# Optimization experiments

Measured on AMD Instinct MI355X. Metric: run time of the kernel, lower is better.

## Reference

```python
import jax, jax.numpy as jnp
import numpy as np

B, C, H, W = 4, 384, 128, 128
HEADS = 8
EPS = 1e-12  # torch F.normalize default eps


def setup_inputs() -> dict:
    key = jax.random.key(0)
    k1, k2, k3, k4 = jax.random.split(key, 4)
    in1 = jax.random.normal(k1, (B, C, H, W), dtype=jnp.float32)
    in2 = jax.random.normal(k2, (B, C, H, W), dtype=jnp.float32)
    temperature = jnp.ones((HEADS, 1, 1), dtype=jnp.float32)
    proj_w = jax.random.normal(k3, (C, C), dtype=jnp.float32) * (1.0 / np.sqrt(C))
    proj_b = jax.random.normal(k4, (C,), dtype=jnp.float32) * 0.01
    return {"in1": in1, "in2": in2, "temperature": temperature,
            "proj_w": proj_w, "proj_b": proj_b}


def _l2norm_last(x):
    # torch F.normalize(dim=-1): x / max(||x||_2, eps)
    n = jnp.sqrt(jnp.sum(x * x, axis=-1, keepdims=True))
    return x / jnp.maximum(n, EPS)


def reference(in1, in2, temperature, proj_w, proj_b):
    b, c, h, w = in1.shape
    hd = c // HEADS  # per-head channels
    # b (head c) h w -> b head c (h w)
    q = in1.reshape(b, HEADS, hd, h * w)
    k = in2.reshape(b, HEADS, hd, h * w)
    q = _l2norm_last(q)
    k = _l2norm_last(k)
    # channel attention: [b, head, hd, hd]
    attn = jnp.einsum('bhcn,bhdn->bhcd', q, k) * temperature[None]
    attn = jax.nn.softmax(attn, axis=-1)
    out = jnp.einsum('bhcd,bhdn->bhcn', attn, k)  # [b, head, hd, HW]
    out = out.reshape(b, c, h, w)
    # 1x1 conv projection
    out = jnp.einsum('oc,bchw->bohw', proj_w, out) + proj_b[None, :, None, None]
    return out
```

## Files before the change

kernel.cpp:

```cpp
#include <hip/hip_runtime.h>
#include <hip/hip_bf16.h>

#define NB 4
#define CC 384
#define HEADS 8
#define HD 48
#define NN 16384
#define NROWS (NB*CC)

typedef __attribute__((ext_vector_type(8))) short bf16x8;
typedef __attribute__((ext_vector_type(4))) float f32x4;

__device__ __forceinline__ unsigned short f2bf(float f) {
  __hip_bfloat16 h = __float2bfloat16(f);
  return __builtin_bit_cast(unsigned short, h);
}

__global__ __launch_bounds__(256) void k_norms(
    const float* __restrict__ in1, const float* __restrict__ in2,
    unsigned short* __restrict__ qbf, unsigned short* __restrict__ kbf)
{
  int row = blockIdx.x;
  bool isK = row >= NROWS;
  int r = isK ? row - NROWS : row;
  const float4* src = (const float4*)((isK ? in2 : in1) + (size_t)r * NN);
  float4 v[16];
  #pragma unroll
  for (int i = 0; i < 16; ++i) v[i] = src[threadIdx.x + i*256];
  float s0 = 0.f, s1 = 0.f, s2 = 0.f, s3 = 0.f;
  #pragma unroll
  for (int i = 0; i < 16; i += 4) {
    s0 += v[i+0].x*v[i+0].x + v[i+0].y*v[i+0].y + v[i+0].z*v[i+0].z + v[i+0].w*v[i+0].w;
    s1 += v[i+1].x*v[i+1].x + v[i+1].y*v[i+1].y + v[i+1].z*v[i+1].z + v[i+1].w*v[i+1].w;
    s2 += v[i+2].x*v[i+2].x + v[i+2].y*v[i+2].y + v[i+2].z*v[i+2].z + v[i+2].w*v[i+2].w;
    s3 += v[i+3].x*v[i+3].x + v[i+3].y*v[i+3].y + v[i+3].z*v[i+3].z + v[i+3].w*v[i+3].w;
  }
  float s = (s0 + s1) + (s2 + s3);
  #pragma unroll
  for (int off = 32; off; off >>= 1) s += __shfl_down(s, off);
  __shared__ float wsum[4];
  __shared__ float rshare;
  if ((threadIdx.x & 63) == 0) wsum[threadIdx.x >> 6] = s;
  __syncthreads();
  if (threadIdx.x == 0) {
    float t = wsum[0] + wsum[1] + wsum[2] + wsum[3];
    rshare = 1.f / fmaxf(sqrtf(t), 1e-12f);
  }
  __syncthreads();
  float rinv = rshare;
  unsigned short* dst = (isK ? kbf : qbf) + (size_t)r * NN;
  #pragma unroll
  for (int i = 0; i < 16; ++i) {
    ushort4 o;
    o.x = f2bf(v[i].x * rinv); o.y = f2bf(v[i].y * rinv);
    o.z = f2bf(v[i].z * rinv); o.w = f2bf(v[i].w * rinv);
    *(ushort4*)(dst + ((size_t)threadIdx.x + i*256) * 4) = o;
  }
}

__global__ __launch_bounds__(256) void k_gram(
    const unsigned short* __restrict__ qbf, const unsigned short* __restrict__ kbf,
    float* __restrict__ partial)
{
  int bh = blockIdx.x;
  int chunk = blockIdx.y;
  int wave = threadIdx.x >> 6, lane = threadIdx.x & 63;
  int b = bh >> 3, h = bh & 7;
  size_t base = ((size_t)(b*CC + h*HD)) * NN;
  int lrow = lane & 15, lk = (lane >> 4) << 3;
  int kstart = chunk*1024 + wave*256;
  f32x4 acc[3][3] = {};
  for (int ks = 0; ks < 8; ++ks) {
    int kpos = kstart + ks*32 + lk;
    bf16x8 a[3], bb[3];
    #pragma unroll
    for (int t = 0; t < 3; ++t) {
      int rr = t*16 + lrow;
      a[t]  = *(const bf16x8*)(qbf + base + (size_t)rr * NN + kpos);
      bb[t] = *(const bf16x8*)(kbf + base + (size_t)rr * NN + kpos);
    }
    #pragma unroll
    for (int i = 0; i < 3; ++i)
      #pragma unroll
      for (int j = 0; j < 3; ++j)
        acc[i][j] = __builtin_amdgcn_mfma_f32_16x16x32_bf16(a[i], bb[j], acc[i][j], 0, 0, 0);
  }
  __shared__ float red[4][HD][HD+1];
  #pragma unroll
  for (int i = 0; i < 3; ++i)
    #pragma unroll
    for (int j = 0; j < 3; ++j)
      #pragma unroll
      for (int m = 0; m < 4; ++m) {
        int rr = i*16 + (lane>>4)*4 + m;
        int cc2 = j*16 + (lane&15);
        red[wave][rr][cc2] = acc[i][j][m];
      }
  __syncthreads();
  float* pout = partial + ((size_t)bh*16 + chunk) * (HD*HD);
  for (int e = threadIdx.x; e < HD*HD; e += 256) {
    int r = e / HD, c = e % HD;
    pout[e] = red[0][r][c] + red[1][r][c] + red[2][r][c] + red[3][r][c];
  }
}

__global__ __launch_bounds__(256) void k_redsm(
    const float* __restrict__ partial, const float* __restrict__ temp,
    float* __restrict__ attn_out)
{
  int bh = blockIdx.x; int h = bh & 7;
  __shared__ float attn[HD][HD+1];
  const float* p = partial + (size_t)bh * 16 * (HD*HD);
  float tscale = temp[h];
  for (int e = threadIdx.x; e < HD*HD; e += 256) {
    float s = 0.f;
    #pragma unroll
    for (int c2 = 0; c2 < 16; ++c2) s += p[c2*(HD*HD) + e];
    attn[e/HD][e%HD] = s * tscale;
  }
  __syncthreads();
  if (threadIdx.x < HD) {
    float* rowp = attn[threadIdx.x];
    float m = rowp[0];
    for (int j = 1; j < HD; ++j) m = fmaxf(m, rowp[j]);
    float sum = 0.f;
    for (int j = 0; j < HD; ++j) { float e = expf(rowp[j]-m); rowp[j] = e; sum += e; }
    float inv = 1.f / sum;
    for (int j = 0; j < HD; ++j) rowp[j] *= inv;
  }
  __syncthreads();
  float* ao = attn_out + (size_t)bh * (HD*HD);
  for (int e = threadIdx.x; e < HD*HD; e += 256)
    ao[e] = attn[e/HD][e%HD];
}

__global__ __launch_bounds__(256) void k_m(
    const float* __restrict__ attn, const float* __restrict__ proj_w,
    unsigned short* __restrict__ Mbf)
{
  int b = blockIdx.x, ot = blockIdx.y;
  int o0 = ot * 16;
  __shared__ float sw[16*CC];
  __shared__ float sa[HEADS*HD*HD];
  const float* ab = attn + (size_t)b * HEADS * HD * HD;
  for (int i = threadIdx.x; i < HEADS*HD*HD; i += 256) sa[i] = ab[i];
  for (int i = threadIdx.x; i < 16*CC; i += 256)
    sw[i] = proj_w[(size_t)(o0 + i/CC)*CC + (i%CC)];
  __syncthreads();
  for (int idx = threadIdx.x; idx < 16*96; idx += 256) {
    int o = idx / 96, c4 = idx % 96;
    int col = c4 * 4;
    int h = col / HD, d = col % HD;
    const float* wp = sw + o*CC + h*HD;
    const float* ap = sa + h*HD*HD + d;
    f32x4 s = {0.f, 0.f, 0.f, 0.f};
    #pragma unroll
    for (int c2 = 0; c2 < HD; ++c2) {
      float w = wp[c2];
      f32x4 av = *(const f32x4*)(ap + c2*HD);
      s += w * av;
    }
    ushort4 o4;
    o4.x = f2bf(s[0]); o4.y = f2bf(s[1]); o4.z = f2bf(s[2]); o4.w = f2bf(s[3]);
    *(ushort4*)(Mbf + ((size_t)b*CC + o0 + o)*CC + col) = o4;
  }
}

#define BM 128
#define BN 128
#define BK 64

__global__ __launch_bounds__(256) void k_final(
    const unsigned short* __restrict__ kbf, const unsigned short* __restrict__ Mbf,
    const float* __restrict__ bias, float* __restrict__ out)
{
  int b = blockIdx.z;
  int bm = blockIdx.y * BM, bn = blockIdx.x * BN;
  int tid = threadIdx.x, lane = tid & 63, wave = tid >> 6;
  int wrow = wave >> 1, wcol = wave & 1;
  __shared__ unsigned short Bt[BN * BK];
  char* btb = (char*)Bt;
  const unsigned short* kb = kbf + (size_t)b * CC * NN;
  const unsigned short* Mb = Mbf + (size_t)b * CC * CC;
  f32x4 acc[4][4] = {};
  int lrow = lane & 15, lkg = lane >> 4;
  for (int k0 = 0; k0 < CC; k0 += BK) {
    #pragma unroll
    for (int s = 0; s < 2; ++s) {
      int slot = tid + s*256;
      int cp = slot >> 4;
      int ng = slot & 15;
      int n0 = ng * 8;
      int c = k0 + cp*2;
      union { uint4 q; unsigned short u[8]; } r0, r1;
      r0.q = *(const uint4*)(kb + (size_t)c*NN + bn + n0);
      r1.q = *(const uint4*)(kb + (size_t)(c+1)*NN + bn + n0);
      #pragma unroll
      for (int i = 0; i < 8; ++i) {
        int n = n0 + i;
        unsigned int val = (unsigned int)r0.u[i] | ((unsigned int)r1.u[i] << 16);
        int pc = (cp>>2) ^ (n & 7) ^ ((n >> 3) & 7);
        *(unsigned int*)(btb + n*128 + (pc<<4) + ((cp&3)<<2)) = val;
      }
    }
    __syncthreads();
    #pragma unroll
    for (int kk = 0; kk < BK; kk += 32) {
      bf16x8 af[4], bfr[4];
      #pragma unroll
      for (int t = 0; t < 4; ++t) {
        int o = bm + wrow*64 + t*16 + lrow;
        af[t] = *(const bf16x8*)(Mb + (size_t)o*CC + (k0 + kk + (lkg<<3)));
        int n = wcol*64 + t*16 + lrow;
        int lc = (kk>>3) + lkg;
        int pc = lc ^ (n & 7) ^ ((n >> 3) & 7);
        bfr[t] = *(const bf16x8*)(btb + n*128 + (pc<<4));
      }
      #pragma unroll
      for (int i = 0; i < 4; ++i)
        #pragma unroll
        for (int j = 0; j < 4; ++j)
          acc[i][j] = __builtin_amdgcn_mfma_f32_16x16x32_bf16(af[i], bfr[j], acc[i][j], 0, 0, 0);
    }
    __syncthreads();
  }
  #pragma unroll
  for (int i = 0; i < 4; ++i) {
    int obase = bm + wrow*64 + i*16 + lkg*4;
    #pragma unroll
    for (int j = 0; j < 4; ++j) {
      int n = bn + wcol*64 + j*16 + lrow;
      #pragma unroll
      for (int m = 0; m < 4; ++m) {
        int o = obase + m;
        out[((size_t)b*CC + o)*NN + n] = acc[i][j][m] + bias[o];
      }
    }
  }
}

extern "C" void kernel_launch(void* const* d_in, const int* in_sizes, int n_in,
                              void* d_out, int out_size, void* d_ws, size_t ws_size,
                              hipStream_t stream)
{
  const float* in1    = (const float*)d_in[0];
  const float* in2    = (const float*)d_in[1];
  const float* temp   = (const float*)d_in[2];
  const float* proj_w = (const float*)d_in[3];
  const float* proj_b = (const float*)d_in[4];
  float* out = (float*)d_out;
  char* ws = (char*)d_ws;

  size_t off = 0;
  unsigned short* qbf = (unsigned short*)(ws + off); off += (size_t)NROWS*NN*2;
  unsigned short* kbf = (unsigned short*)(ws + off); off += (size_t)NROWS*NN*2;
  float* partial  = (float*)(ws + off); off += (size_t)32*16*HD*HD*4;
  float* attn_out = (float*)(ws + off); off += (size_t)32*HD*HD*4;
  unsigned short* Mbf = (unsigned short*)(ws + off);

  k_norms<<<dim3(2*NROWS), dim3(256), 0, stream>>>(in1, in2, qbf, kbf);
  k_gram<<<dim3(32, 16), dim3(256), 0, stream>>>(qbf, kbf, partial);
  k_redsm<<<dim3(32), dim3(256), 0, stream>>>(partial, temp, attn_out);
  k_m<<<dim3(NB, 24), dim3(256), 0, stream>>>(attn_out, proj_w, Mbf);
  k_final<<<dim3(NN/BN, CC/BM, NB), dim3(256), 0, stream>>>(kbf, Mbf, proj_b, out);
}
```

Before: 158.6 us.

## Defer L2 normalization into Gram and projection stages, make conversion a plain copy

The per-row normalization kernel becomes a grid-stride fp32-to-bf16 conversion with no reduction or barriers. Row sum-of-squares are computed from the bf16 values inside the Gram kernel, and the reciprocal norms scale the attention logits and fold into the projection matrix M on the k side. This removes the block-per-row reduction and its synchronization from the bandwidth-bound first pass. In exchange it adds conversion ALU work in the Gram loop, and the norms are now taken from bf16-rounded data rather than fp32.

```diff
diff --git a/kernel.cpp b/kernel.cpp
--- a/kernel.cpp
+++ b/kernel.cpp
@@ -15,52 +15,34 @@
   __hip_bfloat16 h = __float2bfloat16(f);
   return __builtin_bit_cast(unsigned short, h);
 }
-
-__global__ __launch_bounds__(256) void k_norms(
+__device__ __forceinline__ unsigned int packbf(float a, float b) {
+  return (unsigned int)f2bf(a) | ((unsigned int)f2bf(b) << 16);
+}
+__device__ __forceinline__ float bf2f(short s) {
+  unsigned int u = ((unsigned int)(unsigned short)s) << 16;
+  return __builtin_bit_cast(float, u);
+}
+
+__global__ __launch_bounds__(256) void k_copy(
     const float* __restrict__ in1, const float* __restrict__ in2,
     unsigned short* __restrict__ qbf, unsigned short* __restrict__ kbf)
 {
-  int row = blockIdx.x;
-  bool isK = row >= NROWS;
-  int r = isK ? row - NROWS : row;
-  const float4* src = (const float4*)((isK ? in2 : in1) + (size_t)r * NN);
-  float4 v[16];
-  #pragma unroll
-  for (int i = 0; i < 16; ++i) v[i] = src[threadIdx.x + i*256];
-  float s0 = 0.f, s1 = 0.f, s2 = 0.f, s3 = 0.f;
-  #pragma unroll
-  for (int i = 0; i < 16; i += 4) {
-    s0 += v[i+0].x*v[i+0].x + v[i+0].y*v[i+0].y + v[i+0].z*v[i+0].z + v[i+0].w*v[i+0].w;
-    s1 += v[i+1].x*v[i+1].x + v[i+1].y*v[i+1].y + v[i+1].z*v[i+1].z + v[i+1].w*v[i+1].w;
-    s2 += v[i+2].x*v[i+2].x + v[i+2].y*v[i+2].y + v[i+2].z*v[i+2].z + v[i+2].w*v[i+2].w;
-    s3 += v[i+3].x*v[i+3].x + v[i+3].y*v[i+3].y + v[i+3].z*v[i+3].z + v[i+3].w*v[i+3].w;
-  }
-  float s = (s0 + s1) + (s2 + s3);
-  #pragma unroll
-  for (int off = 32; off; off >>= 1) s += __shfl_down(s, off);
-  __shared__ float wsum[4];
-  __shared__ float rshare;
-  if ((threadIdx.x & 63) == 0) wsum[threadIdx.x >> 6] = s;
-  __syncthreads();
-  if (threadIdx.x == 0) {
-    float t = wsum[0] + wsum[1] + wsum[2] + wsum[3];
-    rshare = 1.f / fmaxf(sqrtf(t), 1e-12f);
-  }
-  __syncthreads();
-  float rinv = rshare;
-  unsigned short* dst = (isK ? kbf : qbf) + (size_t)r * NN;
-  #pragma unroll
-  for (int i = 0; i < 16; ++i) {
-    ushort4 o;
-    o.x = f2bf(v[i].x * rinv); o.y = f2bf(v[i].y * rinv);
-    o.z = f2bf(v[i].z * rinv); o.w = f2bf(v[i].w * rinv);
-    *(ushort4*)(dst + ((size_t)threadIdx.x + i*256) * 4) = o;
+  const float4* src = (const float4*)(blockIdx.y ? in2 : in1);
+  uint4* dst = (uint4*)(blockIdx.y ? kbf : qbf);
+  const int n = NROWS * NN / 8;
+  int stride = gridDim.x * 256;
+  for (int i = blockIdx.x * 256 + threadIdx.x; i < n; i += stride) {
+    float4 v0 = src[2*i], v1 = src[2*i+1];
+    uint4 o;
+    o.x = packbf(v0.x, v0.y); o.y = packbf(v0.z, v0.w);
+    o.z = packbf(v1.x, v1.y); o.w = packbf(v1.z, v1.w);
+    dst[i] = o;
   }
 }
 
 __global__ __launch_bounds__(256) void k_gram(
     const unsigned short* __restrict__ qbf, const unsigned short* __restrict__ kbf,
-    float* __restrict__ partial)
+    float* __restrict__ partial, float* __restrict__ sumsq_part)
 {
   int bh = blockIdx.x;
   int chunk = blockIdx.y;
@@ -70,6 +52,7 @@
   int lrow = lane & 15, lk = (lane >> 4) << 3;
   int kstart = chunk*1024 + wave*256;
   f32x4 acc[3][3] = {};
+  float sq[3] = {0.f,0.f,0.f}, sk[3] = {0.f,0.f,0.f};
   for (int ks = 0; ks < 8; ++ks) {
     int kpos = kstart + ks*32 + lk;
     bf16x8 a[3], bb[3];
@@ -80,12 +63,28 @@
       bb[t] = *(const bf16x8*)(kbf + base + (size_t)rr * NN + kpos);
     }
     #pragma unroll
+    for (int t = 0; t < 3; ++t) {
+      #pragma unroll
+      for (int j = 0; j < 8; ++j) {
+        float fa = bf2f(a[t][j]);  sq[t] += fa*fa;
+        float fb = bf2f(bb[t][j]); sk[t] += fb*fb;
+      }
+    }
+    #pragma unroll
     for (int i = 0; i < 3; ++i)
       #pragma unroll
       for (int j = 0; j < 3; ++j)
         acc[i][j] = __builtin_amdgcn_mfma_f32_16x16x32_bf16(a[i], bb[j], acc[i][j], 0, 0, 0);
   }
   __shared__ float red[4][HD][HD+1];
+  __shared__ float sqs[4][96];
+  #pragma unroll
+  for (int t = 0; t < 3; ++t) {
+    float s = sq[t]; s += __shfl_xor(s, 16); s += __shfl_xor(s, 32);
+    if (lane < 16) sqs[wave][t*16 + lane] = s;
+    float s2 = sk[t]; s2 += __shfl_xor(s2, 16); s2 += __shfl_xor(s2, 32);
+    if (lane < 16) sqs[wave][48 + t*16 + lane] = s2;
+  }
   #pragma unroll
   for (int i = 0; i < 3; ++i)
     #pragma unroll
@@ -102,21 +101,38 @@
     int r = e / HD, c = e % HD;
     pout[e] = red[0][r][c] + red[1][r][c] + red[2][r][c] + red[3][r][c];
   }
+  if (threadIdx.x < 96) {
+    float* sout = sumsq_part + ((size_t)bh*16 + chunk) * 96;
+    sout[threadIdx.x] = sqs[0][threadIdx.x] + sqs[1][threadIdx.x]
+                      + sqs[2][threadIdx.x] + sqs[3][threadIdx.x];
+  }
 }
 
 __global__ __launch_bounds__(256) void k_redsm(
-    const float* __restrict__ partial, const float* __restrict__ temp,
-    float* __restrict__ attn_out)
-{
-  int bh = blockIdx.x; int h = bh & 7;
+    const float* __restrict__ partial, const float* __restrict__ sumsq_part,
+    const float* __restrict__ temp, float* __restrict__ attn_out,
+    float* __restrict__ rinv_k_g)
+{
+  int bh = blockIdx.x; int b = bh >> 3, h = bh & 7;
   __shared__ float attn[HD][HD+1];
+  __shared__ float rqs[HD], rks[HD];
+  if (threadIdx.x < 96) {
+    float s = 0.f;
+    #pragma unroll
+    for (int c = 0; c < 16; ++c)
+      s += sumsq_part[((size_t)bh*16 + c)*96 + threadIdx.x];
+    float rinv = 1.f / fmaxf(sqrtf(s), 1e-12f);
+    if (threadIdx.x < 48) rqs[threadIdx.x] = rinv;
+    else { rks[threadIdx.x-48] = rinv; rinv_k_g[b*CC + h*HD + threadIdx.x-48] = rinv; }
+  }
   const float* p = partial + (size_t)bh * 16 * (HD*HD);
   float tscale = temp[h];
+  __syncthreads();
   for (int e = threadIdx.x; e < HD*HD; e += 256) {
     float s = 0.f;
     #pragma unroll
     for (int c2 = 0; c2 < 16; ++c2) s += p[c2*(HD*HD) + e];
-    attn[e/HD][e%HD] = s * tscale;
+    attn[e/HD][e%HD] = s * tscale * rqs[e/HD] * rks[e%HD];
   }
   __syncthreads();
   if (threadIdx.x < HD) {
@@ -136,7 +152,7 @@
 
 __global__ __launch_bounds__(256) void k_m(
     const float* __restrict__ attn, const float* __restrict__ proj_w,
-    unsigned short* __restrict__ Mbf)
+    const float* __restrict__ rinv_k, unsigned short* __restrict__ Mbf)
 {
   int b = blockIdx.x, ot = blockIdx.y;
   int o0 = ot * 16;
@@ -160,6 +176,8 @@
       f32x4 av = *(const f32x4*)(ap + c2*HD);
       s += w * av;
     }
+    f32x4 rk = *(const f32x4*)(rinv_k + b*CC + col);
+    s *= rk;
     ushort4 o4;
     o4.x = f2bf(s[0]); o4.y = f2bf(s[1]); o4.z = f2bf(s[2]); o4.w = f2bf(s[3]);
     *(ushort4*)(Mbf + ((size_t)b*CC + o0 + o)*CC + col) = o4;
@@ -254,13 +272,15 @@
   size_t off = 0;
   unsigned short* qbf = (unsigned short*)(ws + off); off += (size_t)NROWS*NN*2;
   unsigned short* kbf = (unsigned short*)(ws + off); off += (size_t)NROWS*NN*2;
-  float* partial  = (float*)(ws + off); off += (size_t)32*16*HD*HD*4;
-  float* attn_out = (float*)(ws + off); off += (size_t)32*HD*HD*4;
+  float* partial    = (float*)(ws + off); off += (size_t)32*16*HD*HD*4;
+  float* sumsq_part = (float*)(ws + off); off += (size_t)32*16*96*4;
+  float* attn_out   = (float*)(ws + off); off += (size_t)32*HD*HD*4;
+  float* rinv_k     = (float*)(ws + off); off += NROWS*4;
   unsigned short* Mbf = (unsigned short*)(ws + off);
 
-  k_norms<<<dim3(2*NROWS), dim3(256), 0, stream>>>(in1, in2, qbf, kbf);
-  k_gram<<<dim3(32, 16), dim3(256), 0, stream>>>(qbf, kbf, partial);
-  k_redsm<<<dim3(32), dim3(256), 0, stream>>>(partial, temp, attn_out);
-  k_m<<<dim3(NB, 24), dim3(256), 0, stream>>>(attn_out, proj_w, Mbf);
+  k_copy<<<dim3(1024, 2), dim3(256), 0, stream>>>(in1, in2, qbf, kbf);
+  k_gram<<<dim3(32, 16), dim3(256), 0, stream>>>(qbf, kbf, partial, sumsq_part);
+  k_redsm<<<dim3(32), dim3(256), 0, stream>>>(partial, sumsq_part, temp, attn_out, rinv_k);
+  k_m<<<dim3(NB, 24), dim3(256), 0, stream>>>(attn_out, proj_w, rinv_k, Mbf);
   k_final<<<dim3(NN/BN, CC/BM, NB), dim3(256), 0, stream>>>(kbf, Mbf, proj_b, out);
 }
```

Result: no change. 160.1 us (+0.9%).
